# Optimization experiments

Measured on AMD Instinct MI355X. Metric: run time of the kernel, lower is better.

Reference implementation:

```python
import jax, jax.numpy as jnp
import numpy as np

B, S, I, H, O = 32, 4096, 64, 128, 64

def setup_inputs() -> dict:
    key = jax.random.key(0)
    ks = jax.random.split(key, 4)
    xavier_in = float(np.sqrt(6.0 / (I + H)))
    xavier_t3 = float(np.sqrt(6.0 / (H + H * H)))  # xavier_uniform_ on (H, H*H)-shaped fan view of (H,H,H)
    xavier_out = float(np.sqrt(6.0 / (H + O)))
    return {
        "u": jax.random.normal(ks[0], (B, S, I), dtype=jnp.float32),
        "hidden": jnp.zeros((B, H), dtype=jnp.float32),
        "W_in": jax.random.uniform(ks[1], (H, I), dtype=jnp.float32, minval=-xavier_in, maxval=xavier_in),
        "b_in": jnp.zeros((H,), dtype=jnp.float32),
        "T3": jax.random.uniform(ks[2], (H, H, H), dtype=jnp.float32, minval=-xavier_t3, maxval=xavier_t3),
        "bias_t": jnp.zeros((H,), dtype=jnp.float32),
        "W_out": jax.random.uniform(ks[3], (O, H), dtype=jnp.float32, minval=-xavier_out, maxval=xavier_out),
        "b_out": jnp.zeros((O,), dtype=jnp.float32),
    }

def reference(u, hidden, W_in, b_in, T3, bias_t, W_out, b_out):
    # Precompute input projection for all timesteps: [S, B, H]
    input_w = jnp.einsum('bsi,hi->sbh', u, W_in) + b_in

    def step(h, iw_t):
        # bilinear hidden-hidden contraction: out[b,i] = sum_{j,k} h[b,j] T3[i,j,k] h[b,k]
        hw = jnp.einsum('bj,ijk,bk->bi', h, T3, h) + bias_t
        h_new = jnp.tanh(hw + iw_t)
        return h_new, h_new

    h_last, r = jax.lax.scan(step, hidden, input_w)  # r: [S, B, H]
    r_out = jnp.transpose(r, (1, 0, 2))              # [B, S, H]
    output = jnp.einsum('bsh,oh->bso', r_out, W_out) + b_out
    return output, h_last, r_out
```

## Files before the change

kernel.cpp:

```cpp
#include <hip/hip_runtime.h>
#include <math.h>
#include <stdint.h>

#define NB 32
#define NS 4096
#define NI 64
#define NH 128
#define NO 64
#define RT 256

#define CH_STRIDE 12
#define B_STRIDE (16 * CH_STRIDE)

typedef float f4 __attribute__((ext_vector_type(4)));
typedef unsigned int u4 __attribute__((ext_vector_type(4)));

__global__ __launch_bounds__(256)
void k_input_proj(const float* __restrict__ u, const float* __restrict__ W_in,
                  const float* __restrict__ b_in, float* __restrict__ iw)
{
    const int gid = blockIdx.x * 256 + threadIdx.x;
    const int h = gid & (NH - 1);
    const int t = (gid >> 7) & (NS - 1);
    const int b = gid >> 19;
    const f4* ur = reinterpret_cast<const f4*>(u + ((size_t)b * NS + t) * NI);
    const f4* wr = reinterpret_cast<const f4*>(W_in + h * NI);
    float acc = b_in[h];
#pragma unroll
    for (int q = 0; q < NI / 4; ++q) {
        const f4 uv = ur[q], wv = wr[q];
        acc = fmaf(uv[0], wv[0], acc); acc = fmaf(uv[1], wv[1], acc);
        acc = fmaf(uv[2], wv[2], acc); acc = fmaf(uv[3], wv[3], acc);
    }
    iw[gid] = acc;
}

__global__ __launch_bounds__(256)
void k_init_hex(const float* __restrict__ hidden, uint64_t* __restrict__ hex)
{
    const int gid = blockIdx.x * 256 + threadIdx.x;
    const int b = gid & (NB - 1);
    const int i = gid >> 5;
    hex[gid] = (uint64_t)__float_as_uint(hidden[b * NH + i]);
}

__global__ __launch_bounds__(RT)
__attribute__((amdgpu_waves_per_eu(1, 1)))
void k_recur(const float* __restrict__ T3, const float* __restrict__ bias_t,
             float* __restrict__ r_region,
             float* __restrict__ h_last,
             uint64_t* hex)
{
    const int bi  = blockIdx.x;
    const int i   = bi >> 1;
    const int bh  = bi & 1;
    const int B0  = bh * 16;
    const int tid = threadIdx.x;
    const int jg  = tid >> 4;
    const int kg  = tid & 15;
    const int w   = tid >> 6;

    const int ipol = tid >> 1;
    const int oct  = 2 * bh + (tid & 1);
    const int bl0  = (tid & 1) * 8;

    __shared__ float h_lds[16 * B_STRIDE];
    __shared__ float redbuf[4][16];
    __shared__ float lds_pad[20480];

    const float* base = T3 + (size_t)i * NH * NH + (size_t)(jg * 8) * NH + kg * 8;
    f4 t3_0, t3_1, t3_2, t3_3, t3_4, t3_5, t3_6, t3_7;
    f4 t3_8, t3_9, t3_10, t3_11, t3_12, t3_13, t3_14, t3_15;
#define T3LOAD(dst, fofs) \
    asm volatile("global_load_dwordx4 %0, %1, off" \
                 : "=v"(dst) : "v"(base + (fofs)) : "memory")
    T3LOAD(t3_0,  0 * NH);     T3LOAD(t3_1,  0 * NH + 4);
    T3LOAD(t3_2,  1 * NH);     T3LOAD(t3_3,  1 * NH + 4);
    T3LOAD(t3_4,  2 * NH);     T3LOAD(t3_5,  2 * NH + 4);
    T3LOAD(t3_6,  3 * NH);     T3LOAD(t3_7,  3 * NH + 4);
    T3LOAD(t3_8,  4 * NH);     T3LOAD(t3_9,  4 * NH + 4);
    T3LOAD(t3_10, 5 * NH);     T3LOAD(t3_11, 5 * NH + 4);
    T3LOAD(t3_12, 6 * NH);     T3LOAD(t3_13, 6 * NH + 4);
    T3LOAD(t3_14, 7 * NH);     T3LOAD(t3_15, 7 * NH + 4);
#undef T3LOAD
    asm volatile("s_waitcnt vmcnt(0)" ::: "memory");
    __builtin_amdgcn_sched_barrier(0);

    const float bias = bias_t[i];
    if (bias > 1.0e30f) lds_pad[tid] = bias;

    float iw_cur = 0.f;
    if (tid < 16)
        iw_cur = r_region[((size_t)(B0 + tid) * NS + 0) * NH + i];

    for (int t = 0; t < NS; ++t) {
        {
            const uint64_t* src = hex + ((size_t)(t & 1) * NH + ipol) * NB + oct * 8;
            u4 q0, q1, q2, q3;
            const uint32_t et = (uint32_t)t;
            for (;;) {
                asm volatile(
                    "global_load_dwordx4 %0, %4, off sc0 sc1\n\t"
                    "global_load_dwordx4 %1, %4, off offset:16 sc0 sc1\n\t"
                    "global_load_dwordx4 %2, %4, off offset:32 sc0 sc1\n\t"
                    "global_load_dwordx4 %3, %4, off offset:48 sc0 sc1\n\t"
                    "s_waitcnt vmcnt(0)"
                    : "=&v"(q0), "=&v"(q1), "=&v"(q2), "=&v"(q3)
                    : "v"(src) : "memory");
                if (q0[1] == et && q0[3] == et && q1[1] == et && q1[3] == et &&
                    q2[1] == et && q2[3] == et && q3[1] == et && q3[3] == et)
                    break;
            }
            float* dst = h_lds + bl0 * B_STRIDE
                       + (ipol >> 3) * CH_STRIDE + (ipol & 7);
            dst[0 * B_STRIDE] = __uint_as_float(q0[0]);
            dst[1 * B_STRIDE] = __uint_as_float(q0[2]);
            dst[2 * B_STRIDE] = __uint_as_float(q1[0]);
            dst[3 * B_STRIDE] = __uint_as_float(q1[2]);
            dst[4 * B_STRIDE] = __uint_as_float(q2[0]);
            dst[5 * B_STRIDE] = __uint_as_float(q2[2]);
            dst[6 * B_STRIDE] = __uint_as_float(q3[0]);
            dst[7 * B_STRIDE] = __uint_as_float(q3[2]);
        }
        __syncthreads();

#define JJBODY(tA, tB, HJV) \
        { float s0 = 0.f, s1 = 0.f; \
          s0 = fmaf(tA[0], hk0[0], s0); s1 = fmaf(tA[1], hk0[1], s1); \
          s0 = fmaf(tA[2], hk0[2], s0); s1 = fmaf(tA[3], hk0[3], s1); \
          s0 = fmaf(tB[0], hk1[0], s0); s1 = fmaf(tB[1], hk1[1], s1); \
          s0 = fmaf(tB[2], hk1[2], s0); s1 = fmaf(tB[3], hk1[3], s1); \
          acc = fmaf(HJV, s0 + s1, acc); }
#pragma unroll 4
        for (int b = 0; b < 16; ++b) {
            const float* row = h_lds + b * B_STRIDE;
            const f4 hj0 = *reinterpret_cast<const f4*>(row + jg * CH_STRIDE);
            const f4 hj1 = *reinterpret_cast<const f4*>(row + jg * CH_STRIDE + 4);
            const f4 hk0 = *reinterpret_cast<const f4*>(row + kg * CH_STRIDE);
            const f4 hk1 = *reinterpret_cast<const f4*>(row + kg * CH_STRIDE + 4);
            float acc = 0.f;
            JJBODY(t3_0,  t3_1,  hj0[0]);
            JJBODY(t3_2,  t3_3,  hj0[1]);
            JJBODY(t3_4,  t3_5,  hj0[2]);
            JJBODY(t3_6,  t3_7,  hj0[3]);
            JJBODY(t3_8,  t3_9,  hj1[0]);
            JJBODY(t3_10, t3_11, hj1[1]);
            JJBODY(t3_12, t3_13, hj1[2]);
            JJBODY(t3_14, t3_15, hj1[3]);
            acc += __shfl_xor(acc, 1);  acc += __shfl_xor(acc, 2);
            acc += __shfl_xor(acc, 4);  acc += __shfl_xor(acc, 8);
            acc += __shfl_xor(acc, 16); acc += __shfl_xor(acc, 32);
            if ((tid & 63) == b) redbuf[w][b] = acc;
        }
#undef JJBODY
        __syncthreads();

        if (tid < 16) {
            const int b = B0 + tid;
            const float s = redbuf[0][tid] + redbuf[1][tid]
                          + redbuf[2][tid] + redbuf[3][tid];
            const float hn = tanhf(s + bias + iw_cur);
            const uint64_t pv = ((uint64_t)(uint32_t)(t + 1) << 32)
                              | (uint64_t)__float_as_uint(hn);
            uint64_t* dstp = hex + ((size_t)((t + 1) & 1) * NH + i) * NB + b;
            asm volatile("global_store_dwordx2 %0, %1, off sc0 sc1"
                         :: "v"(dstp), "v"(pv) : "memory");
            const size_t ridx = ((size_t)b * NS + t) * NH + i;
            r_region[ridx] = hn;
            if (t + 1 < NS) iw_cur = r_region[ridx + NH];
            if (t == NS - 1) h_last[(size_t)b * NH + i] = hn;
        }
    }
}

__global__ __launch_bounds__(256)
void k_out_proj(const float* __restrict__ r, const float* __restrict__ W_out,
                const float* __restrict__ b_out, float* __restrict__ out)
{
    const int gid = blockIdx.x * 256 + threadIdx.x;
    const int o = gid & (NO - 1);
    const int s = (gid >> 6) & (NS - 1);
    const int b = gid >> 18;
    const f4* rr = reinterpret_cast<const f4*>(r + ((size_t)b * NS + s) * NH);
    const f4* wr = reinterpret_cast<const f4*>(W_out + o * NH);
    float acc = b_out[o];
#pragma unroll
    for (int q = 0; q < NH / 4; ++q) {
        const f4 rv = rr[q], wv = wr[q];
        acc = fmaf(rv[0], wv[0], acc); acc = fmaf(rv[1], wv[1], acc);
        acc = fmaf(rv[2], wv[2], acc); acc = fmaf(rv[3], wv[3], acc);
    }
    out[gid] = acc;
}

extern "C" void kernel_launch(void* const* d_in, const int* in_sizes, int n_in,
                              void* d_out, int out_size, void* d_ws, size_t ws_size,
                              hipStream_t stream)
{
    const float* u      = (const float*)d_in[0];
    const float* hidden = (const float*)d_in[1];
    const float* W_in   = (const float*)d_in[2];
    const float* b_in   = (const float*)d_in[3];
    const float* T3     = (const float*)d_in[4];
    const float* bias_t = (const float*)d_in[5];
    const float* W_out  = (const float*)d_in[6];
    const float* b_out  = (const float*)d_in[7];

    float* out_f  = (float*)d_out;
    float* out_y  = out_f;
    float* out_hl = out_f + (size_t)NB * NS * NO;
    float* out_r  = out_hl + (size_t)NB * NH;

    uint64_t* hex = (uint64_t*)d_ws;

    hipMemsetAsync(hex, 0xFF, 2 * NB * NH * sizeof(uint64_t), stream);
    k_init_hex<<<(NB * NH) / 256, 256, 0, stream>>>(hidden, hex);

    k_input_proj<<<(NB * NS * NH) / 256, 256, 0, stream>>>(u, W_in, b_in, out_r);
    k_recur<<<2 * NH, RT, 0, stream>>>(T3, bias_t, out_r, out_hl, hex);
    k_out_proj<<<(NB * NS * NO) / 256, 256, 0, stream>>>(out_r, W_out, b_out, out_y);
}
```

Before: 38.28 ms.

## Split recurrent step into four batch groups with per-group flag wait and publish

The time loop of the persistent recurrent kernel now runs as four sub-steps, each over four batch rows. Every sub-step waits only for the flagged hidden values of its own rows, computes their bilinear contraction, and publishes the new hidden state for those rows immediately. Other blocks can then start on early batch groups while later groups are still in flight, pipelining the cross-block exchange. The cost is two extra barriers per group, so eight per step instead of two, plus an s_sleep in the spin-wait that adds latency when polling.

```diff
diff --git a/kernel.cpp b/kernel.cpp
--- a/kernel.cpp
+++ b/kernel.cpp
@@ -61,8 +61,7 @@
     const int w   = tid >> 6;
 
     const int ipol = tid >> 1;
-    const int oct  = 2 * bh + (tid & 1);
-    const int bl0  = (tid & 1) * 8;
+    const int pp   = tid & 1;
 
     __shared__ float h_lds[16 * B_STRIDE];
     __shared__ float redbuf[4][16];
@@ -93,37 +92,6 @@
     if (tid < 16)
         iw_cur = r_region[((size_t)(B0 + tid) * NS + 0) * NH + i];
 
-    for (int t = 0; t < NS; ++t) {
-        {
-            const uint64_t* src = hex + ((size_t)(t & 1) * NH + ipol) * NB + oct * 8;
-            u4 q0, q1, q2, q3;
-            const uint32_t et = (uint32_t)t;
-            for (;;) {
-                asm volatile(
-                    "global_load_dwordx4 %0, %4, off sc0 sc1\n\t"
-                    "global_load_dwordx4 %1, %4, off offset:16 sc0 sc1\n\t"
-                    "global_load_dwordx4 %2, %4, off offset:32 sc0 sc1\n\t"
-                    "global_load_dwordx4 %3, %4, off offset:48 sc0 sc1\n\t"
-                    "s_waitcnt vmcnt(0)"
-                    : "=&v"(q0), "=&v"(q1), "=&v"(q2), "=&v"(q3)
-                    : "v"(src) : "memory");
-                if (q0[1] == et && q0[3] == et && q1[1] == et && q1[3] == et &&
-                    q2[1] == et && q2[3] == et && q3[1] == et && q3[3] == et)
-                    break;
-            }
-            float* dst = h_lds + bl0 * B_STRIDE
-                       + (ipol >> 3) * CH_STRIDE + (ipol & 7);
-            dst[0 * B_STRIDE] = __uint_as_float(q0[0]);
-            dst[1 * B_STRIDE] = __uint_as_float(q0[2]);
-            dst[2 * B_STRIDE] = __uint_as_float(q1[0]);
-            dst[3 * B_STRIDE] = __uint_as_float(q1[2]);
-            dst[4 * B_STRIDE] = __uint_as_float(q2[0]);
-            dst[5 * B_STRIDE] = __uint_as_float(q2[2]);
-            dst[6 * B_STRIDE] = __uint_as_float(q3[0]);
-            dst[7 * B_STRIDE] = __uint_as_float(q3[2]);
-        }
-        __syncthreads();
-
 #define JJBODY(tA, tB, HJV) \
         { float s0 = 0.f, s1 = 0.f; \
           s0 = fmaf(tA[0], hk0[0], s0); s1 = fmaf(tA[1], hk0[1], s1); \
@@ -131,46 +99,71 @@
           s0 = fmaf(tB[0], hk1[0], s0); s1 = fmaf(tB[1], hk1[1], s1); \
           s0 = fmaf(tB[2], hk1[2], s0); s1 = fmaf(tB[3], hk1[3], s1); \
           acc = fmaf(HJV, s0 + s1, acc); }
-#pragma unroll 4
-        for (int b = 0; b < 16; ++b) {
-            const float* row = h_lds + b * B_STRIDE;
-            const f4 hj0 = *reinterpret_cast<const f4*>(row + jg * CH_STRIDE);
-            const f4 hj1 = *reinterpret_cast<const f4*>(row + jg * CH_STRIDE + 4);
-            const f4 hk0 = *reinterpret_cast<const f4*>(row + kg * CH_STRIDE);
-            const f4 hk1 = *reinterpret_cast<const f4*>(row + kg * CH_STRIDE + 4);
-            float acc = 0.f;
-            JJBODY(t3_0,  t3_1,  hj0[0]);
-            JJBODY(t3_2,  t3_3,  hj0[1]);
-            JJBODY(t3_4,  t3_5,  hj0[2]);
-            JJBODY(t3_6,  t3_7,  hj0[3]);
-            JJBODY(t3_8,  t3_9,  hj1[0]);
-            JJBODY(t3_10, t3_11, hj1[1]);
-            JJBODY(t3_12, t3_13, hj1[2]);
-            JJBODY(t3_14, t3_15, hj1[3]);
-            acc += __shfl_xor(acc, 1);  acc += __shfl_xor(acc, 2);
-            acc += __shfl_xor(acc, 4);  acc += __shfl_xor(acc, 8);
-            acc += __shfl_xor(acc, 16); acc += __shfl_xor(acc, 32);
-            if ((tid & 63) == b) redbuf[w][b] = acc;
-        }
-#undef JJBODY
-        __syncthreads();
-
-        if (tid < 16) {
-            const int b = B0 + tid;
-            const float s = redbuf[0][tid] + redbuf[1][tid]
-                          + redbuf[2][tid] + redbuf[3][tid];
-            const float hn = tanhf(s + bias + iw_cur);
-            const uint64_t pv = ((uint64_t)(uint32_t)(t + 1) << 32)
-                              | (uint64_t)__float_as_uint(hn);
-            uint64_t* dstp = hex + ((size_t)((t + 1) & 1) * NH + i) * NB + b;
-            asm volatile("global_store_dwordx2 %0, %1, off sc0 sc1"
-                         :: "v"(dstp), "v"(pv) : "memory");
-            const size_t ridx = ((size_t)b * NS + t) * NH + i;
-            r_region[ridx] = hn;
-            if (t + 1 < NS) iw_cur = r_region[ridx + NH];
-            if (t == NS - 1) h_last[(size_t)b * NH + i] = hn;
+
+    for (int t = 0; t < NS; ++t) {
+        const uint32_t et = (uint32_t)t;
+#pragma unroll
+        for (int g = 0; g < 4; ++g) {
+            {
+                const uint64_t* src = hex + ((size_t)(t & 1) * NH + ipol) * NB
+                                    + B0 + g * 4 + 2 * pp;
+                u4 q;
+                for (;;) {
+                    asm volatile("global_load_dwordx4 %0, %1, off sc0 sc1\n\t"
+                                 "s_waitcnt vmcnt(0)"
+                                 : "=v"(q) : "v"(src) : "memory");
+                    if (q[1] == et && q[3] == et) break;
+                    asm volatile("s_sleep 1");
+                }
+                float* dst = h_lds + (g * 4 + 2 * pp) * B_STRIDE
+                           + (ipol >> 3) * CH_STRIDE + (ipol & 7);
+                dst[0]        = __uint_as_float(q[0]);
+                dst[B_STRIDE] = __uint_as_float(q[2]);
+            }
+            __syncthreads();
+
+#pragma unroll
+            for (int rr = 0; rr < 4; ++rr) {
+                const int row = g * 4 + rr;
+                const float* hrow = h_lds + row * B_STRIDE;
+                const f4 hj0 = *reinterpret_cast<const f4*>(hrow + jg * CH_STRIDE);
+                const f4 hj1 = *reinterpret_cast<const f4*>(hrow + jg * CH_STRIDE + 4);
+                const f4 hk0 = *reinterpret_cast<const f4*>(hrow + kg * CH_STRIDE);
+                const f4 hk1 = *reinterpret_cast<const f4*>(hrow + kg * CH_STRIDE + 4);
+                float acc = 0.f;
+                JJBODY(t3_0,  t3_1,  hj0[0]);
+                JJBODY(t3_2,  t3_3,  hj0[1]);
+                JJBODY(t3_4,  t3_5,  hj0[2]);
+                JJBODY(t3_6,  t3_7,  hj0[3]);
+                JJBODY(t3_8,  t3_9,  hj1[0]);
+                JJBODY(t3_10, t3_11, hj1[1]);
+                JJBODY(t3_12, t3_13, hj1[2]);
+                JJBODY(t3_14, t3_15, hj1[3]);
+                acc += __shfl_xor(acc, 1);  acc += __shfl_xor(acc, 2);
+                acc += __shfl_xor(acc, 4);  acc += __shfl_xor(acc, 8);
+                acc += __shfl_xor(acc, 16); acc += __shfl_xor(acc, 32);
+                if ((tid & 63) == row) redbuf[w][row] = acc;
+            }
+            __syncthreads();
+
+            if ((tid >> 2) == g) {
+                const int b = B0 + tid;
+                const float s = redbuf[0][tid] + redbuf[1][tid]
+                              + redbuf[2][tid] + redbuf[3][tid];
+                const float hn = tanhf(s + bias + iw_cur);
+                const uint64_t pv = ((uint64_t)(uint32_t)(t + 1) << 32)
+                                  | (uint64_t)__float_as_uint(hn);
+                uint64_t* dstp = hex + ((size_t)((t + 1) & 1) * NH + i) * NB + b;
+                asm volatile("global_store_dwordx2 %0, %1, off sc0 sc1"
+                             :: "v"(dstp), "v"(pv) : "memory");
+                const size_t ridx = ((size_t)b * NS + t) * NH + i;
+                r_region[ridx] = hn;
+                if (t + 1 < NS) iw_cur = r_region[ridx + NH];
+                if (t == NS - 1) h_last[(size_t)b * NH + i] = hn;
+            }
         }
     }
+#undef JJBODY
 }
 
 __global__ __launch_bounds__(256)
```

Measured after the change: 39.49 ms. +3.1%, slower.
